# Performance work log

Hardware: AMD Instinct MI355X
Metric: run time of the kernel (lower is better)

The kernel has to match this reference:

```python
import jax, jax.numpy as jnp
import numpy as np

B, H, W = 4, 1024, 1024

# 8-tap Sobel-style stencil: offsets in (u, v) units of (dx, dy)
OFF_U = jnp.array([-1.0, -1.0, -1.0, 0.0, 0.0, 1.0, 1.0, 1.0], dtype=jnp.float32)
OFF_V = jnp.array([-1.0, 0.0, 1.0, -1.0, 1.0, -1.0, 0.0, 1.0], dtype=jnp.float32)
KU = jnp.array([-0.25, -0.5, -0.25, 0.0, 0.0, 0.25, 0.5, 0.25], dtype=jnp.float32)
KV = jnp.array([-0.25, 0.0, 0.25, -0.5, 0.5, -0.25, 0.0, 0.25], dtype=jnp.float32)


def setup_inputs() -> dict:
    key = jax.random.key(0)
    k1, k2 = jax.random.split(key)
    x = jax.random.uniform(k1, (B, 3, H, W), dtype=jnp.float32)
    sigma = jax.random.uniform(k2, (B,), dtype=jnp.float32) * 2.0 + 0.5  # pixels
    return {"x": x, "sigma": sigma}


def _bilinear(tex, u, v):
    # tex: [3, H, W]; u, v: [8, H, W] normalized UV in [0,1]
    Hh, Ww = tex.shape[1], tex.shape[2]
    px = u * Ww - 0.5
    py = v * Hh - 0.5
    x0 = jnp.floor(px)
    y0 = jnp.floor(py)
    fx = (px - x0)[None]  # [1,8,H,W]
    fy = (py - y0)[None]
    x0i = jnp.clip(x0.astype(jnp.int32), 0, Ww - 1)
    x1i = jnp.clip(x0i + 1, 0, Ww - 1)
    y0i = jnp.clip(y0.astype(jnp.int32), 0, Hh - 1)
    y1i = jnp.clip(y0i + 1, 0, Hh - 1)
    t00 = tex[:, y0i, x0i]  # [3,8,H,W]
    t01 = tex[:, y0i, x1i]
    t10 = tex[:, y1i, x0i]
    t11 = tex[:, y1i, x1i]
    return (t00 * (1 - fx) * (1 - fy) + t01 * fx * (1 - fy)
            + t10 * (1 - fx) * fy + t11 * fx * fy)


def reference(x, sigma):
    Bb, C, Hh, Ww = x.shape
    ys, xs = jnp.meshgrid(jnp.arange(Hh, dtype=x.dtype),
                          jnp.arange(Ww, dtype=x.dtype), indexing='ij')
    u0 = (xs + 0.5) / Ww  # pixel-center UV
    v0 = (ys + 0.5) / Hh
    dx = sigma / Ww  # [B]
    dy = sigma / Hh
    u = u0[None, None] + OFF_U[None, :, None, None] * dx[:, None, None, None]  # [B,8,H,W]
    v = v0[None, None] + OFF_V[None, :, None, None] * dy[:, None, None, None]
    s = jax.vmap(_bilinear)(x, u, v)  # [B,3,8,H,W]
    s_u = jnp.einsum('bcthw,t->bchw', s, KU)
    s_v = jnp.einsum('bcthw,t->bchw', s, KV)
    lum = jnp.array([100.0, 1.0, 1.0], dtype=x.dtype)[None, :, None, None]
    s_u = s_u * lum
    s_v = s_v * lum
    # structure tensor components E, G, F
    return jnp.stack([(s_u * s_u).sum(1), (s_v * s_v).sum(1), (s_u * s_v).sum(1)], axis=1)
```

## Files before the change

### kernel.cpp

```cpp
#include <hip/hip_runtime.h>


#define W_ 1024
#define H_ 1024
#define PLANE (1 << 20)
#define ROWS 4

__device__ __forceinline__ float lerp1(float a, float b, float f) {
    return fmaf(f, b - a, a);
}

__device__ void slow_pixel(const float* __restrict__ Xb, float* __restrict__ Ob,
                           float sg, int xi, int y)
{
    float imf = floorf(-sg), ipf = floorf(sg);
    float fm  = -sg - imf;
    float fp  =  sg - ipf;
    int   im  = (int)imf, ip = (int)ipf;

    int cm0 = min(max(xi + im, 0), W_ - 1), cm1 = min(cm0 + 1, W_ - 1);
    int cp0 = min(max(xi + ip, 0), W_ - 1), cp1 = min(cp0 + 1, W_ - 1);
    int rm0 = min(max(y + im, 0), H_ - 1),  rm1 = min(rm0 + 1, H_ - 1);
    int rp0 = min(max(y + ip, 0), H_ - 1),  rp1 = min(rp0 + 1, H_ - 1);

    int o_rm0 = rm0 << 10, o_rm1 = rm1 << 10;
    int o_rp0 = rp0 << 10, o_rp1 = rp1 << 10;
    int o_r0  = y   << 10;

    float oxx = 0.f, oyy = 0.f, oxy = 0.f;

    #pragma unroll
    for (int c = 0; c < 3; ++c) {
        const float* base = Xb + ((size_t)c << 20);

        float hm_m0 = lerp1(base[o_rm0 + cm0], base[o_rm0 + cm1], fm);
        float hm_m1 = lerp1(base[o_rm1 + cm0], base[o_rm1 + cm1], fm);
        float hm_0  = lerp1(base[o_r0  + cm0], base[o_r0  + cm1], fm);
        float hm_p0 = lerp1(base[o_rp0 + cm0], base[o_rp0 + cm1], fm);
        float hm_p1 = lerp1(base[o_rp1 + cm0], base[o_rp1 + cm1], fm);
        float hp_m0 = lerp1(base[o_rm0 + cp0], base[o_rm0 + cp1], fp);
        float hp_m1 = lerp1(base[o_rm1 + cp0], base[o_rm1 + cp1], fp);
        float hp_0  = lerp1(base[o_r0  + cp0], base[o_r0  + cp1], fp);
        float hp_p0 = lerp1(base[o_rp0 + cp0], base[o_rp0 + cp1], fp);
        float hp_p1 = lerp1(base[o_rp1 + cp0], base[o_rp1 + cp1], fp);
        float h0_m0 = base[o_rm0 + xi], h0_m1 = base[o_rm1 + xi];
        float h0_p0 = base[o_rp0 + xi], h0_p1 = base[o_rp1 + xi];

        float t0 = lerp1(hm_m0, hm_m1, fm);
        float t1 = hm_0;
        float t2 = lerp1(hm_p0, hm_p1, fp);
        float t3 = lerp1(h0_m0, h0_m1, fm);
        float t4 = lerp1(h0_p0, h0_p1, fp);
        float t5 = lerp1(hp_m0, hp_m1, fm);
        float t6 = hp_0;
        float t7 = lerp1(hp_p0, hp_p1, fp);

        float su = 0.25f * (t5 + t7 - t0 - t2) + 0.5f * (t6 - t1);
        float sv = 0.25f * (t2 + t7 - t0 - t5) + 0.5f * (t4 - t3);

        float l2 = (c == 0) ? 10000.f : 1.f;
        oxx = fmaf(l2 * su, su, oxx);
        oyy = fmaf(l2 * sv, sv, oyy);
        oxy = fmaf(l2 * su, sv, oxy);
    }

    int pix = (y << 10) | xi;
    Ob[pix]             = oxx;
    Ob[PLANE + pix]     = oyy;
    Ob[2 * PLANE + pix] = oxy;
}

template<int N>
__device__ __forceinline__ void acc(float (&arr)[N], int k, float val) {
    if (k >= 0 && k < N) arr[k] += val;
}

template<int IP>
__device__ void fast4(const float* __restrict__ Xb, float* __restrict__ Ob,
                      float fp, float fm, int x, int y0)
{
    constexpr int RW = ROWS + 2 * IP + 2;

    int cm0 = max(x - (IP + 1), 0);
    int cm1 = cm0 + 1;
    int cp0 = min(x + IP, W_ - 1);
    int cp1 = min(cp0 + 1, W_ - 1);

    float oxx[ROWS], oyy[ROWS], oxy[ROWS];
    #pragma unroll
    for (int k = 0; k < ROWS; ++k) { oxx[k] = 0.f; oyy[k] = 0.f; oxy[k] = 0.f; }

    #pragma unroll
    for (int c = 0; c < 3; ++c) {
        const float* base = Xb + ((size_t)c << 20) + ((y0 - IP - 1) << 10);
        float su[ROWS], sv[ROWS];
        #pragma unroll
        for (int k = 0; k < ROWS; ++k) { su[k] = 0.f; sv[k] = 0.f; }

        #pragma unroll
        for (int w = 0; w < RW; ++w) {
            const float* rp = base + (w << 10);
            float a0 = rp[cm0], a1 = rp[cm1];
            float b0 = rp[cp0], b1 = rp[cp1];
            float cc = rp[x];
            float hm = lerp1(a0, a1, fm);
            float hp = lerp1(b0, b1, fp);
            float q  = hp - hm;
            float A  = 0.25f * q;
            float hq = 0.5f  * q;
            float Bv = fmaf(0.25f, hm + hp, 0.5f * cc);
            float fpA = fp * A, fmA = fm * A;
            float fpB = fp * Bv, fmB = fm * Bv;

            acc(su, w,              fpA);
            acc(su, w - 1,          fmA);
            acc(su, w - IP - 1,     hq);
            acc(su, w - 2*IP - 1,   fmA);
            acc(su, w - 2*IP - 2,   fpA);
            acc(sv, w,             -fpB);
            acc(sv, w - 1,         -fmB);
            acc(sv, w - 2*IP - 1,   fmB);
            acc(sv, w - 2*IP - 2,   fpB);
        }

        float l2 = (c == 0) ? 10000.f : 1.f;
        #pragma unroll
        for (int k = 0; k < ROWS; ++k) {
            oxx[k] = fmaf(l2 * su[k], su[k], oxx[k]);
            oyy[k] = fmaf(l2 * sv[k], sv[k], oyy[k]);
            oxy[k] = fmaf(l2 * su[k], sv[k], oxy[k]);
        }
    }

    #pragma unroll
    for (int k = 0; k < ROWS; ++k) {
        int pix = ((y0 + k) << 10) | x;
        Ob[pix]             = oxx[k];
        Ob[PLANE + pix]     = oyy[k];
        Ob[2 * PLANE + pix] = oxy[k];
    }
}

__global__ __launch_bounds__(256) void st_kernel(
    const float* __restrict__ X, const float* __restrict__ S,
    float* __restrict__ O)
{
    int x  = blockIdx.x * 64 + threadIdx.x;
    int y0 = blockIdx.y * 16 + threadIdx.y * ROWS;
    int b  = blockIdx.z;

    const float* Xb = X + (size_t)b * 3 * PLANE;
    float*       Ob = O + (size_t)b * 3 * PLANE;
    float sg = S[b];

    int ip = (int)floorf(sg);
    int im = (int)floorf(-sg);
    bool sig_ok = (im == -ip - 1) && ip >= 0 && ip <= 2;
    bool fast   = sig_ok && (y0 - ip - 1 >= 0) && (y0 + ROWS + ip <= H_ - 1);

    float fp = sg - (float)ip;
    float fm = 1.0f - fp;

    if (fast) {
        switch (ip) {
            case 0:  fast4<0>(Xb, Ob, fp, fm, x, y0); break;
            case 1:  fast4<1>(Xb, Ob, fp, fm, x, y0); break;
            default: fast4<2>(Xb, Ob, fp, fm, x, y0); break;
        }
    } else {
        for (int k = 0; k < ROWS; ++k)
            slow_pixel(Xb, Ob, sg, x, y0 + k);
    }
}

extern "C" void kernel_launch(void* const* d_in, const int* in_sizes, int n_in,
                              void* d_out, int out_size, void* d_ws, size_t ws_size,
                              hipStream_t stream) {
    const float* x     = (const float*)d_in[0];
    const float* sigma = (const float*)d_in[1];
    float* out = (float*)d_out;

    dim3 grid(W_ / 64, H_ / 16, 4), block(64, 4);
    hipLaunchKernelGGL(st_kernel, grid, block, 0, stream, x, sigma, out);
}
```

Measured before the change: 117.9 us.

## Compute two columns per thread with float2 loads and separate border blocks

Each thread now computes two adjacent output columns, loading row windows with float2 vector loads and writing results as float2 stores, which halves the thread count and shares loaded neighbours between the two columns. Border pixels (edge rows and the outer columns) are no longer handled inline. They are moved to an extra row of blocks that runs the slow bilinear path, so the fast path can use clamped row and column offsets without per-thread branching. This adds per-thread register pressure and a small serial tail of border blocks.

```diff
diff --git a/kernel.cpp b/kernel.cpp
--- a/kernel.cpp
+++ b/kernel.cpp
@@ -76,68 +76,115 @@
 }
 
 template<int IP>
-__device__ void fast4(const float* __restrict__ Xb, float* __restrict__ Ob,
+__device__ void fast2(const float* __restrict__ Xb, float* __restrict__ Ob,
                       float fp, float fm, int x, int y0)
 {
-    constexpr int RW = ROWS + 2 * IP + 2;
-
-    int cm0 = max(x - (IP + 1), 0);
-    int cm1 = cm0 + 1;
-    int cp0 = min(x + IP, W_ - 1);
-    int cp1 = min(cp0 + 1, W_ - 1);
-
-    float oxx[ROWS], oyy[ROWS], oxy[ROWS];
-    #pragma unroll
-    for (int k = 0; k < ROWS; ++k) { oxx[k] = 0.f; oyy[k] = 0.f; oxy[k] = 0.f; }
+    constexpr int RW   = ROWS + 2 * IP + 2;
+    constexpr int OFFS = (IP == 2) ? 4 : 2;
+    constexpr int NW2  = (IP == 2) ? 5 : 3;
+    constexpr int NW   = 2 * NW2;
+    constexpr int E0   = (IP == 1) ? 0 : 1;
+    constexpr int E1   = IP + OFFS;
+    constexpr int EC   = OFFS;
+
+    int goff[NW2];
+    #pragma unroll
+    for (int g = 0; g < NW2; ++g)
+        goff[g] = min(max(x - OFFS + 2 * g, 0), W_ - 2);
+
+    int rown[RW];
+    #pragma unroll
+    for (int w = 0; w < RW; ++w)
+        rown[w] = min(max(y0 - IP - 1 + w, 0), H_ - 1) << 10;
+
+    float oxx0[ROWS], oyy0[ROWS], oxy0[ROWS];
+    float oxx1[ROWS], oyy1[ROWS], oxy1[ROWS];
+    #pragma unroll
+    for (int k = 0; k < ROWS; ++k) {
+        oxx0[k] = 0.f; oyy0[k] = 0.f; oxy0[k] = 0.f;
+        oxx1[k] = 0.f; oyy1[k] = 0.f; oxy1[k] = 0.f;
+    }
 
     #pragma unroll
     for (int c = 0; c < 3; ++c) {
-        const float* base = Xb + ((size_t)c << 20) + ((y0 - IP - 1) << 10);
-        float su[ROWS], sv[ROWS];
-        #pragma unroll
-        for (int k = 0; k < ROWS; ++k) { su[k] = 0.f; sv[k] = 0.f; }
+        const float* base = Xb + ((size_t)c << 20);
+        float su0[ROWS], sv0[ROWS], su1[ROWS], sv1[ROWS];
+        #pragma unroll
+        for (int k = 0; k < ROWS; ++k) {
+            su0[k] = 0.f; sv0[k] = 0.f; su1[k] = 0.f; sv1[k] = 0.f;
+        }
 
         #pragma unroll
         for (int w = 0; w < RW; ++w) {
-            const float* rp = base + (w << 10);
-            float a0 = rp[cm0], a1 = rp[cm1];
-            float b0 = rp[cp0], b1 = rp[cp1];
-            float cc = rp[x];
-            float hm = lerp1(a0, a1, fm);
-            float hp = lerp1(b0, b1, fp);
-            float q  = hp - hm;
-            float A  = 0.25f * q;
-            float hq = 0.5f  * q;
-            float Bv = fmaf(0.25f, hm + hp, 0.5f * cc);
-            float fpA = fp * A, fmA = fm * A;
-            float fpB = fp * Bv, fmB = fm * Bv;
-
-            acc(su, w,              fpA);
-            acc(su, w - 1,          fmA);
-            acc(su, w - IP - 1,     hq);
-            acc(su, w - 2*IP - 1,   fmA);
-            acc(su, w - 2*IP - 2,   fpA);
-            acc(sv, w,             -fpB);
-            acc(sv, w - 1,         -fmB);
-            acc(sv, w - 2*IP - 1,   fmB);
-            acc(sv, w - 2*IP - 2,   fpB);
+            const float* rp = base + rown[w];
+            float wv[NW];
+            #pragma unroll
+            for (int g = 0; g < NW2; ++g) {
+                float2 L = *reinterpret_cast<const float2*>(rp + goff[g]);
+                wv[2 * g]     = L.x;
+                wv[2 * g + 1] = L.y;
+            }
+
+            float hm0 = lerp1(wv[E0],     wv[E0 + 1], fm);
+            float hm1 = lerp1(wv[E0 + 1], wv[E0 + 2], fm);
+            float hp0 = lerp1(wv[E1],     wv[E1 + 1], fp);
+            float hp1 = lerp1(wv[E1 + 1], wv[E1 + 2], fp);
+            float cc0 = wv[EC], cc1 = wv[EC + 1];
+
+            float q0  = hp0 - hm0,      q1  = hp1 - hm1;
+            float A0  = 0.25f * q0,     A1  = 0.25f * q1;
+            float hq0 = 0.5f  * q0,     hq1 = 0.5f  * q1;
+            float B0  = fmaf(0.25f, hm0 + hp0, 0.5f * cc0);
+            float B1  = fmaf(0.25f, hm1 + hp1, 0.5f * cc1);
+            float fpA0 = fp * A0, fmA0 = fm * A0, fpB0 = fp * B0, fmB0 = fm * B0;
+            float fpA1 = fp * A1, fmA1 = fm * A1, fpB1 = fp * B1, fmB1 = fm * B1;
+
+            acc(su0, w,              fpA0);  acc(su1, w,              fpA1);
+            acc(su0, w - 1,          fmA0);  acc(su1, w - 1,          fmA1);
+            acc(su0, w - IP - 1,     hq0);   acc(su1, w - IP - 1,     hq1);
+            acc(su0, w - 2*IP - 1,   fmA0);  acc(su1, w - 2*IP - 1,   fmA1);
+            acc(su0, w - 2*IP - 2,   fpA0);  acc(su1, w - 2*IP - 2,   fpA1);
+            acc(sv0, w,             -fpB0);  acc(sv1, w,             -fpB1);
+            acc(sv0, w - 1,         -fmB0);  acc(sv1, w - 1,         -fmB1);
+            acc(sv0, w - 2*IP - 1,   fmB0);  acc(sv1, w - 2*IP - 1,   fmB1);
+            acc(sv0, w - 2*IP - 2,   fpB0);  acc(sv1, w - 2*IP - 2,   fpB1);
         }
 
         float l2 = (c == 0) ? 10000.f : 1.f;
         #pragma unroll
         for (int k = 0; k < ROWS; ++k) {
-            oxx[k] = fmaf(l2 * su[k], su[k], oxx[k]);
-            oyy[k] = fmaf(l2 * sv[k], sv[k], oyy[k]);
-            oxy[k] = fmaf(l2 * su[k], sv[k], oxy[k]);
-        }
-    }
-
+            oxx0[k] = fmaf(l2 * su0[k], su0[k], oxx0[k]);
+            oyy0[k] = fmaf(l2 * sv0[k], sv0[k], oyy0[k]);
+            oxy0[k] = fmaf(l2 * su0[k], sv0[k], oxy0[k]);
+            oxx1[k] = fmaf(l2 * su1[k], su1[k], oxx1[k]);
+            oyy1[k] = fmaf(l2 * sv1[k], sv1[k], oyy1[k]);
+            oxy1[k] = fmaf(l2 * su1[k], sv1[k], oxy1[k]);
+        }
+    }
+
+    bool okx0 = (x     > IP) && (x     < W_ - 1 - IP);
+    bool okx1 = (x + 1 > IP) && (x + 1 < W_ - 1 - IP);
     #pragma unroll
     for (int k = 0; k < ROWS; ++k) {
-        int pix = ((y0 + k) << 10) | x;
-        Ob[pix]             = oxx[k];
-        Ob[PLANE + pix]     = oyy[k];
-        Ob[2 * PLANE + pix] = oxy[k];
+        if (y0 + k > IP) {
+            int pix = ((y0 + k) << 10) | x;
+            if (okx0 && okx1) {
+                *reinterpret_cast<float2*>(Ob + pix)             = make_float2(oxx0[k], oxx1[k]);
+                *reinterpret_cast<float2*>(Ob + PLANE + pix)     = make_float2(oyy0[k], oyy1[k]);
+                *reinterpret_cast<float2*>(Ob + 2 * PLANE + pix) = make_float2(oxy0[k], oxy1[k]);
+            } else {
+                if (okx0) {
+                    Ob[pix]             = oxx0[k];
+                    Ob[PLANE + pix]     = oyy0[k];
+                    Ob[2 * PLANE + pix] = oxy0[k];
+                }
+                if (okx1) {
+                    Ob[pix + 1]             = oxx1[k];
+                    Ob[PLANE + pix + 1]     = oyy1[k];
+                    Ob[2 * PLANE + pix + 1] = oxy1[k];
+                }
+            }
+        }
     }
 }
 
@@ -145,31 +192,49 @@
     const float* __restrict__ X, const float* __restrict__ S,
     float* __restrict__ O)
 {
-    int x  = blockIdx.x * 64 + threadIdx.x;
-    int y0 = blockIdx.y * 16 + threadIdx.y * ROWS;
     int b  = blockIdx.z;
-
     const float* Xb = X + (size_t)b * 3 * PLANE;
     float*       Ob = O + (size_t)b * 3 * PLANE;
     float sg = S[b];
 
-    int ip = (int)floorf(sg);
-    int im = (int)floorf(-sg);
-    bool sig_ok = (im == -ip - 1) && ip >= 0 && ip <= 2;
-    bool fast   = sig_ok && (y0 - ip - 1 >= 0) && (y0 + ROWS + ip <= H_ - 1);
-
-    float fp = sg - (float)ip;
+    if (blockIdx.y == (H_ / 16)) {
+        int tid = blockIdx.x * 256 + threadIdx.y * 64 + threadIdx.x;
+        #pragma unroll
+        for (int it = 0; it < 5; ++it) {
+            int pidx = tid + it * 2048;
+            if (pidx < 6144) {
+                int yy = pidx / 6;
+                int cc = pidx - yy * 6;
+                int xx = (cc < 3) ? cc : (W_ - 6 + cc);
+                slow_pixel(Xb, Ob, sg, xx, yy);
+            } else if (pidx < 9216) {
+                int p2 = pidx - 6144;
+                slow_pixel(Xb, Ob, sg, p2 & 1023, p2 >> 10);
+            }
+        }
+        return;
+    }
+
+    int x  = blockIdx.x * 128 + threadIdx.x * 2;
+    int y0 = blockIdx.y * 16 + threadIdx.y * ROWS;
+
+    int ipv = (int)floorf(sg);
+    int imv = (int)floorf(-sg);
+    bool sig_ok = (imv == -ipv - 1) && ipv >= 0 && ipv <= 2;
+    float fp = sg - (float)ipv;
     float fm = 1.0f - fp;
 
-    if (fast) {
-        switch (ip) {
-            case 0:  fast4<0>(Xb, Ob, fp, fm, x, y0); break;
-            case 1:  fast4<1>(Xb, Ob, fp, fm, x, y0); break;
-            default: fast4<2>(Xb, Ob, fp, fm, x, y0); break;
+    if (sig_ok) {
+        switch (ipv) {
+            case 0:  fast2<0>(Xb, Ob, fp, fm, x, y0); break;
+            case 1:  fast2<1>(Xb, Ob, fp, fm, x, y0); break;
+            default: fast2<2>(Xb, Ob, fp, fm, x, y0); break;
         }
     } else {
-        for (int k = 0; k < ROWS; ++k)
-            slow_pixel(Xb, Ob, sg, x, y0 + k);
+        for (int k = 0; k < ROWS; ++k) {
+            slow_pixel(Xb, Ob, sg, x,     y0 + k);
+            slow_pixel(Xb, Ob, sg, x + 1, y0 + k);
+        }
     }
 }
 
@@ -180,6 +245,6 @@
     const float* sigma = (const float*)d_in[1];
     float* out = (float*)d_out;
 
-    dim3 grid(W_ / 64, H_ / 16, 4), block(64, 4);
+    dim3 grid(W_ / 128, H_ / 16 + 1, 4), block(64, 4);
     hipLaunchKernelGGL(st_kernel, grid, block, 0, stream, x, sigma, out);
 }
```

Result: slower. 136.0 us (+15.3%).

## Stage input tiles in shared memory with float4 loads and move borders to separate blocks

Applied to the files above, without the earlier changes.

Each block now covers a 64x32 output tile. For each channel it cooperatively loads the needed input rows, with halo, into LDS using vectorized float4 loads, and the stencil then reads from LDS instead of global memory. Each thread computes 8 rows instead of 4. Border columns and the top rows are handled by an extra row of blocks that runs the slow per-pixel path. This cuts redundant global and cache traffic, at the cost of barriers per channel and lower occupancy from the LDS use.

```diff
diff --git a/kernel.cpp b/kernel.cpp
--- a/kernel.cpp
+++ b/kernel.cpp
@@ -4,7 +4,10 @@
 #define W_ 1024
 #define H_ 1024
 #define PLANE (1 << 20)
-#define ROWS 4
+#define TCOLS 64
+#define TROWS 32
+#define ROWS 8
+#define LSTRIDE 72
 
 __device__ __forceinline__ float lerp1(float a, float b, float f) {
     return fmaf(f, b - a, a);
@@ -76,40 +79,54 @@
 }
 
 template<int IP>
-__device__ void fast4(const float* __restrict__ Xb, float* __restrict__ Ob,
-                      float fp, float fm, int x, int y0)
+__device__ void fast_tile(const float* __restrict__ Xb, float* __restrict__ Ob,
+                          float fp, float fm, int x0, int y0,
+                          int tx, int ty, int tid, float* smem)
 {
-    constexpr int RW = ROWS + 2 * IP + 2;
-
-    int cm0 = max(x - (IP + 1), 0);
-    int cm1 = cm0 + 1;
-    int cp0 = min(x + IP, W_ - 1);
-    int cp1 = min(cp0 + 1, W_ - 1);
+    constexpr int LROWS = TROWS + 2 * IP + 2;
+    constexpr int RW    = ROWS + 2 * IP + 2;
+    constexpr int NG    = LROWS * 18;
+
+    int x = x0 + tx;
+    int Y = y0 + ty * ROWS;
 
     float oxx[ROWS], oyy[ROWS], oxy[ROWS];
     #pragma unroll
     for (int k = 0; k < ROWS; ++k) { oxx[k] = 0.f; oyy[k] = 0.f; oxy[k] = 0.f; }
 
-    #pragma unroll
+    const float* sp = smem + (ty * ROWS) * LSTRIDE + tx + (3 - IP);
+
     for (int c = 0; c < 3; ++c) {
-        const float* base = Xb + ((size_t)c << 20) + ((y0 - IP - 1) << 10);
+        const float* Xc = Xb + ((size_t)c << 20);
+
+        for (int g = tid; g < NG; g += 256) {
+            int row = g / 18;
+            int grp = g - row * 18;
+            int gr  = min(max(y0 - IP - 1 + row, 0), H_ - 1);
+            int gc  = min(max(x0 - 4 + grp * 4, 0), W_ - 4);
+            *reinterpret_cast<float4*>(&smem[row * LSTRIDE + grp * 4]) =
+                *reinterpret_cast<const float4*>(&Xc[(gr << 10) + gc]);
+        }
+        __syncthreads();
+
         float su[ROWS], sv[ROWS];
         #pragma unroll
         for (int k = 0; k < ROWS; ++k) { su[k] = 0.f; sv[k] = 0.f; }
 
         #pragma unroll
         for (int w = 0; w < RW; ++w) {
-            const float* rp = base + (w << 10);
-            float a0 = rp[cm0], a1 = rp[cm1];
-            float b0 = rp[cp0], b1 = rp[cp1];
-            float cc = rp[x];
+            float a0 = sp[w * LSTRIDE];
+            float a1 = sp[w * LSTRIDE + 1];
+            float cc = sp[w * LSTRIDE + IP + 1];
+            float b0 = sp[w * LSTRIDE + 2 * IP + 1];
+            float b1 = sp[w * LSTRIDE + 2 * IP + 2];
             float hm = lerp1(a0, a1, fm);
             float hp = lerp1(b0, b1, fp);
             float q  = hp - hm;
             float A  = 0.25f * q;
             float hq = 0.5f  * q;
             float Bv = fmaf(0.25f, hm + hp, 0.5f * cc);
-            float fpA = fp * A, fmA = fm * A;
+            float fpA = fp * A,  fmA = fm * A;
             float fpB = fp * Bv, fmB = fm * Bv;
 
             acc(su, w,              fpA);
@@ -130,14 +147,19 @@
             oyy[k] = fmaf(l2 * sv[k], sv[k], oyy[k]);
             oxy[k] = fmaf(l2 * su[k], sv[k], oxy[k]);
         }
-    }
-
+        __syncthreads();
+    }
+
+    bool okx = (x > IP) && (x < W_ - 1 - IP);
     #pragma unroll
     for (int k = 0; k < ROWS; ++k) {
-        int pix = ((y0 + k) << 10) | x;
-        Ob[pix]             = oxx[k];
-        Ob[PLANE + pix]     = oyy[k];
-        Ob[2 * PLANE + pix] = oxy[k];
+        int y = Y + k;
+        if (okx && y > IP) {
+            int pix = (y << 10) | x;
+            Ob[pix]             = oxx[k];
+            Ob[PLANE + pix]     = oyy[k];
+            Ob[2 * PLANE + pix] = oxy[k];
+        }
     }
 }
 
@@ -145,31 +167,52 @@
     const float* __restrict__ X, const float* __restrict__ S,
     float* __restrict__ O)
 {
-    int x  = blockIdx.x * 64 + threadIdx.x;
-    int y0 = blockIdx.y * 16 + threadIdx.y * ROWS;
     int b  = blockIdx.z;
-
     const float* Xb = X + (size_t)b * 3 * PLANE;
     float*       Ob = O + (size_t)b * 3 * PLANE;
     float sg = S[b];
 
-    int ip = (int)floorf(sg);
-    int im = (int)floorf(-sg);
-    bool sig_ok = (im == -ip - 1) && ip >= 0 && ip <= 2;
-    bool fast   = sig_ok && (y0 - ip - 1 >= 0) && (y0 + ROWS + ip <= H_ - 1);
-
-    float fp = sg - (float)ip;
+    int tx = threadIdx.x, ty = threadIdx.y;
+    int tid = ty * 64 + tx;
+
+    if (blockIdx.y == (H_ / TROWS)) {
+        int t = blockIdx.x * 256 + tid;
+        #pragma unroll
+        for (int it = 0; it < 3; ++it) {
+            int pidx = t + it * 4096;
+            if (pidx < 6144) {
+                int yy = pidx / 6;
+                int cc = pidx - yy * 6;
+                int xx = (cc < 3) ? cc : (W_ - 6 + cc);
+                slow_pixel(Xb, Ob, sg, xx, yy);
+            } else if (pidx < 9216) {
+                int p2 = pidx - 6144;
+                slow_pixel(Xb, Ob, sg, p2 & 1023, p2 >> 10);
+            }
+        }
+        return;
+    }
+
+    int x0 = blockIdx.x * TCOLS;
+    int y0 = blockIdx.y * TROWS;
+
+    int ipv = (int)floorf(sg);
+    int imv = (int)floorf(-sg);
+    bool sig_ok = (imv == -ipv - 1) && ipv >= 0 && ipv <= 2;
+    float fp = sg - (float)ipv;
     float fm = 1.0f - fp;
 
-    if (fast) {
-        switch (ip) {
-            case 0:  fast4<0>(Xb, Ob, fp, fm, x, y0); break;
-            case 1:  fast4<1>(Xb, Ob, fp, fm, x, y0); break;
-            default: fast4<2>(Xb, Ob, fp, fm, x, y0); break;
+    __shared__ float smem[(TROWS + 6) * LSTRIDE];
+
+    if (sig_ok) {
+        switch (ipv) {
+            case 0:  fast_tile<0>(Xb, Ob, fp, fm, x0, y0, tx, ty, tid, smem); break;
+            case 1:  fast_tile<1>(Xb, Ob, fp, fm, x0, y0, tx, ty, tid, smem); break;
+            default: fast_tile<2>(Xb, Ob, fp, fm, x0, y0, tx, ty, tid, smem); break;
         }
     } else {
         for (int k = 0; k < ROWS; ++k)
-            slow_pixel(Xb, Ob, sg, x, y0 + k);
+            slow_pixel(Xb, Ob, sg, x0 + tx, y0 + ty * ROWS + k);
     }
 }
 
@@ -180,6 +223,6 @@
     const float* sigma = (const float*)d_in[1];
     float* out = (float*)d_out;
 
-    dim3 grid(W_ / 64, H_ / 16, 4), block(64, 4);
+    dim3 grid(W_ / TCOLS, H_ / TROWS + 1, 4), block(64, 4);
     hipLaunchKernelGGL(st_kernel, grid, block, 0, stream, x, sigma, out);
 }
```

After: 117.6 us. Within noise of the previous version (-0.3%).
